# Performance work log

Hardware: AMD Instinct MI355X
Metric: run time of the kernel (lower is better)

## Reference

```python
import jax, jax.numpy as jnp
import numpy as np

B, T, D = 4, 2048, 1024
H, HS = 16, 64  # n_head, head_size


def setup_inputs() -> dict:
    key = jax.random.key(0)
    ks = jax.random.split(key, 6)
    s_in = 1.0 / np.sqrt(D)
    s_out = 1.0 / np.sqrt(H * HS)
    x = jax.random.normal(ks[0], (B, T, D), dtype=jnp.float32)
    Wq = jax.random.uniform(ks[1], (H, D, HS), jnp.float32, -s_in, s_in)
    Wk = jax.random.uniform(ks[2], (H, D, HS), jnp.float32, -s_in, s_in)
    Wv = jax.random.uniform(ks[3], (H, D, HS), jnp.float32, -s_in, s_in)
    Wo = jax.random.uniform(ks[4], (H * HS, D), jnp.float32, -s_out, s_out)
    bo = jax.random.uniform(ks[5], (D,), jnp.float32, -s_out, s_out)
    return {"x": x, "Wq": Wq, "Wk": Wk, "Wv": Wv, "Wo": Wo, "bo": bo}


def reference(x, Wq, Wk, Wv, Wo, bo):
    # per-head projections, batched across heads: [B,T,D] x [H,D,HS] -> [B,H,T,HS]
    q = jnp.einsum("btd,hde->bhte", x, Wq)
    k = jnp.einsum("btd,hde->bhte", x, Wk)
    v = jnp.einsum("btd,hde->bhte", x, Wv)
    scale = HS ** -0.5
    scores = jnp.einsum("bhqe,bhke->bhqk", q, k) * scale  # [B,H,T,T]
    causal = jnp.tril(jnp.ones((T, T), dtype=bool))
    scores = jnp.where(causal, scores, jnp.float32(-jnp.inf))
    attn = jax.nn.softmax(scores, axis=-1)
    out = jnp.einsum("bhqk,bhke->bhqe", attn, v)  # [B,H,T,HS]
    out = out.transpose(0, 2, 1, 3).reshape(B, T, H * HS)  # concat heads
    return out @ Wo + bo
```

## Files before the change

kernel.cpp:

```cpp
#include <hip/hip_runtime.h>

typedef __attribute__((ext_vector_type(8))) short short8v;
typedef __attribute__((ext_vector_type(4))) short short4v;
typedef __attribute__((ext_vector_type(4))) float floatx4;
typedef __attribute__((ext_vector_type(4))) unsigned uint4v;
typedef __attribute__((ext_vector_type(2))) unsigned long long ulong2v;

namespace {
constexpr int Bn = 4, Tn = 2048, Dn = 1024, Hn = 16, HSn = 64;
}

__device__ __forceinline__ short f2bf(float f) {
  unsigned u = __builtin_bit_cast(unsigned, f);
  u += 0x7fffu + ((u >> 16) & 1u);
  return (short)(u >> 16);
}

__device__ __forceinline__ unsigned pkbf2(float lo, float hi) {
  unsigned r;
  asm("v_cvt_pk_bf16_f32 %0, %1, %2" : "=v"(r) : "v"(lo), "v"(hi));
  return r;
}

typedef const __attribute__((address_space(1))) unsigned int guint_t;
typedef __attribute__((address_space(3))) unsigned int luint_t;

__device__ __forceinline__ void gload16(const void* g, void* l) {
  __builtin_amdgcn_global_load_lds((guint_t*)g, (luint_t*)l, 16, 0, 0);
}

__device__ __forceinline__ short8v rd8(const char* base, int row, int kel) {
  return *(const short8v*)(base + row * 128 + ((kel * 2) ^ ((row & 7) << 4)));
}

__global__ __launch_bounds__(256) void cvt_x_k(const float* __restrict__ x, short* __restrict__ xb) {
  const size_t i = ((size_t)blockIdx.x * 256 + threadIdx.x) * 8;
  const float4 a = *(const float4*)(x + i);
  const float4 b = *(const float4*)(x + i + 4);
  short8v o;
  o[0] = f2bf(a.x); o[1] = f2bf(a.y); o[2] = f2bf(a.z); o[3] = f2bf(a.w);
  o[4] = f2bf(b.x); o[5] = f2bf(b.y); o[6] = f2bf(b.z); o[7] = f2bf(b.w);
  *(short8v*)(xb + i) = o;
}

__global__ __launch_bounds__(256) void tr_w_k(const float* __restrict__ Wq, const float* __restrict__ Wk,
                                              const float* __restrict__ Wv, const float* __restrict__ Wo,
                                              short* __restrict__ wt, short* __restrict__ wot) {
  __shared__ float T[64][65];
  const int t = threadIdx.x;
  const int rr = t >> 2, c0 = (t & 3) * 4;
  const float* src;
  short* dst;
  if (blockIdx.x < 48) {
    const int ph = blockIdx.x;
    const int p = ph >> 4, h = ph & 15;
    const int dt = blockIdx.y;
    const float* W = p == 0 ? Wq : p == 1 ? Wk : Wv;
    src = W + (size_t)h * (Dn * HSn) + (size_t)(dt * 64 + rr) * HSn;
    dst = wt + ((size_t)p * 1024 + h * 64 + rr) * 1024 + dt * 64;
  } else {
    const int ktile = blockIdx.x - 48, ntile = blockIdx.y;
    src = Wo + (size_t)(ktile * 64 + rr) * Dn + ntile * 64;
    dst = wot + (size_t)(ntile * 64 + rr) * 1024 + ktile * 64;
  }
  #pragma unroll
  for (int q = 0; q < 4; ++q) {
    const float4 v = *(const float4*)(src + c0 + q * 16);
    T[rr][c0 + q * 16 + 0] = v.x; T[rr][c0 + q * 16 + 1] = v.y;
    T[rr][c0 + q * 16 + 2] = v.z; T[rr][c0 + q * 16 + 3] = v.w;
  }
  __syncthreads();
  #pragma unroll
  for (int q = 0; q < 4; ++q) {
    const int dl = c0 + q * 16;
    short4v ov = {f2bf(T[dl + 0][rr]), f2bf(T[dl + 1][rr]),
                  f2bf(T[dl + 2][rr]), f2bf(T[dl + 3][rr])};
    *(short4v*)(dst + dl) = ov;
  }
}

__device__ __forceinline__ void gemm_mainloop(const char* gA, const char* gB, char* As, char* Bs,
                                              floatx4 acc[4][4]) {
  const int tid = threadIdx.x;
  const int wv = tid >> 6, ln = tid & 63;
  const int wr = wv >> 1, wc = wv & 1;
  const int lr = ln >> 3, lg = ln & 7;
  const int fr = ln & 15, kq = ln >> 4;
  for (int kt = 0; kt < 16; ++kt) {
    __syncthreads();
    #pragma unroll
    for (int c = 0; c < 4; ++c) {
      const int r = wv * 32 + c * 8 + lr;
      const int sw = (lg * 16) ^ ((r & 7) * 16);
      gload16(gA + (size_t)r * 2048 + kt * 128 + sw, As + (wv * 32 + c * 8) * 128);
      gload16(gB + (size_t)r * 2048 + kt * 128 + sw, Bs + (wv * 32 + c * 8) * 128);
    }
    __syncthreads();
    #pragma unroll
    for (int kb = 0; kb < 2; ++kb) {
      const int k0 = kb * 32 + kq * 8;
      short8v af[4], bfr[4];
      #pragma unroll
      for (int i = 0; i < 4; ++i) af[i] = rd8(As, wr * 64 + i * 16 + fr, k0);
      #pragma unroll
      for (int j = 0; j < 4; ++j) bfr[j] = rd8(Bs, wc * 64 + j * 16 + fr, k0);
      #pragma unroll
      for (int i = 0; i < 4; ++i)
        #pragma unroll
        for (int j = 0; j < 4; ++j)
          acc[i][j] = __builtin_amdgcn_mfma_f32_16x16x32_bf16(af[i], bfr[j], acc[i][j], 0, 0, 0);
    }
  }
}

__global__ __launch_bounds__(256) void gemm_qkv_k(const short* __restrict__ xb, const short* __restrict__ wt,
                                                  short* __restrict__ qb, short* __restrict__ kb,
                                                  short* __restrict__ vb) {
  __shared__ __align__(16) char As[16384];
  __shared__ __align__(16) char Bs[16384];
  const int m0 = blockIdx.x * 128, n0 = blockIdx.y * 128;
  floatx4 acc[4][4];
  #pragma unroll
  for (int i = 0; i < 4; ++i)
    #pragma unroll
    for (int j = 0; j < 4; ++j) acc[i][j] = floatx4{0.f, 0.f, 0.f, 0.f};
  gemm_mainloop((const char*)xb + (size_t)m0 * 2048, (const char*)wt + (size_t)n0 * 2048, As, Bs, acc);

  const int tid = threadIdx.x, wv = tid >> 6, ln = tid & 63;
  const int wr = wv >> 1, wc = wv & 1;
  const int proj = n0 >> 10;
  const int b = m0 >> 11;
  const int rb_ = (ln >> 4) * 4, fc = ln & 15;
  if (proj < 2) {
    short* dst = proj == 0 ? qb : kb;
    const float sc = proj == 0 ? 0.18033688011112042f : 1.0f;
    #pragma unroll
    for (int i = 0; i < 4; ++i) {
      const int m = m0 + wr * 64 + i * 16 + rb_;
      #pragma unroll
      for (int j = 0; j < 4; ++j) {
        const int n = n0 + wc * 64 + j * 16 + fc;
        const int h = (n >> 6) & 15, e = n & 63;
        short* dp = dst + ((size_t)(b * 16 + h) * Tn + (m & 2047)) * 64 + e;
        #pragma unroll
        for (int r = 0; r < 4; ++r) dp[(size_t)r * 64] = f2bf(acc[i][j][r] * sc);
      }
    }
  } else {
    #pragma unroll
    for (int i = 0; i < 4; ++i) {
      const int m = m0 + wr * 64 + i * 16 + rb_;
      const int t0 = m & 2047;
      #pragma unroll
      for (int j = 0; j < 4; ++j) {
        const int n = n0 + wc * 64 + j * 16 + fc;
        const int h = (n >> 6) & 15, e = n & 63;
        short4v ov = {f2bf(acc[i][j][0]), f2bf(acc[i][j][1]),
                      f2bf(acc[i][j][2]), f2bf(acc[i][j][3])};
        *(short4v*)(vb + ((size_t)(b * 16 + h) * 64 + e) * Tn + t0) = ov;
      }
    }
  }
}

__global__ __launch_bounds__(256, 4) void attn_k(const short* __restrict__ qg, const short* __restrict__ kg,
                                                 const short* __restrict__ vg, short* __restrict__ og) {
  __shared__ __align__(16) char Ks[16384];
  __shared__ __align__(16) char Vs[16384];
  const int qt = gridDim.y - 1 - blockIdx.y;
  const int bh = blockIdx.x;
  const int tid = threadIdx.x, wv = tid >> 6, ln = tid & 63;
  const int lr = ln >> 3, lg = ln & 7;
  const int fr = ln & 15, kq = ln >> 4;
  const char* qbase = (const char*)qg + (size_t)bh * Tn * 128;
  const char* kbase = (const char*)kg + (size_t)bh * Tn * 128;
  const char* vbase = (const char*)vg + (size_t)bh * Tn * 128;

  #pragma unroll
  for (int c = 0; c < 2; ++c) {
    const int r = c * 32 + wv * 8 + lr;
    const int sw = (lg * 16) ^ ((r & 7) * 16);
    gload16(kbase + (size_t)r * 128 + sw, Ks + (c * 32 + wv * 8) * 128);
    gload16(vbase + (size_t)r * 4096 + sw, Vs + (c * 32 + wv * 8) * 128);
  }

  const char* qrow0 = qbase + (size_t)(qt * 128 + wv * 32) * 128;
  short8v qf[2][2];
  #pragma unroll
  for (int c = 0; c < 2; ++c)
    #pragma unroll
    for (int kb = 0; kb < 2; ++kb)
      qf[c][kb] = *(const short8v*)(qrow0 + (c * 16 + fr) * 128 + kb * 64 + kq * 16);

  short8v ones8;
  #pragma unroll
  for (int i = 0; i < 8; ++i) ones8[i] = (short)0x3F80;

  floatx4 ot[4][2];
  #pragma unroll
  for (int f = 0; f < 4; ++f) { ot[f][0] = floatx4{0.f,0.f,0.f,0.f}; ot[f][1] = floatx4{0.f,0.f,0.f,0.f}; }
  floatx4 lacc[2] = {floatx4{0.f,0.f,0.f,0.f}, floatx4{0.f,0.f,0.f,0.f}};
  float m_i[2] = {-1e30f, -1e30f};

  const int swz = (fr & 7) * 16;
  const int nkt = 2 * qt + 2;
  const int q0w = qt * 128 + wv * 32;
  __syncthreads();

  for (int kt = 0; kt < nkt; ++kt) {
    const int cur = kt & 1;
    if (kt + 1 < nkt) {
      #pragma unroll
      for (int c = 0; c < 2; ++c) {
        const int r = c * 32 + wv * 8 + lr;
        const int sw = (lg * 16) ^ ((r & 7) * 16);
        gload16(kbase + (size_t)((kt + 1) * 64 + r) * 128 + sw,
                Ks + (cur ^ 1) * 8192 + (c * 32 + wv * 8) * 128);
        gload16(vbase + (size_t)r * 4096 + (size_t)(kt + 1) * 128 + sw,
                Vs + (cur ^ 1) * 8192 + (c * 32 + wv * 8) * 128);
      }
    }
    if (kt * 64 <= q0w + 31) {
      const char* Ksc = Ks + cur * 8192;
      const char* Vsc = Vs + cur * 8192;
      floatx4 st[2][4];
      #pragma unroll
      for (int f = 0; f < 4; ++f) { st[0][f] = floatx4{0.f,0.f,0.f,0.f}; st[1][f] = floatx4{0.f,0.f,0.f,0.f}; }
      #pragma unroll
      for (int kb = 0; kb < 2; ++kb) {
        const int e0 = kb * 32 + kq * 8;
        #pragma unroll
        for (int f = 0; f < 4; ++f) {
          const short8v kf = rd8(Ksc, f * 16 + fr, e0);
          st[0][f] = __builtin_amdgcn_mfma_f32_16x16x32_bf16(kf, qf[0][kb], st[0][f], 0, 0, 0);
          st[1][f] = __builtin_amdgcn_mfma_f32_16x16x32_bf16(kf, qf[1][kb], st[1][f], 0, 0, 0);
        }
      }
      if (kt * 64 + 63 > q0w) {
        #pragma unroll
        for (int c = 0; c < 2; ++c) {
          const int q = q0w + c * 16 + fr;
          #pragma unroll
          for (int f = 0; f < 4; ++f)
            #pragma unroll
            for (int r = 0; r < 4; ++r)
              if (kt * 64 + f * 16 + kq * 4 + r > q) st[c][f][r] = -3.0e38f;
        }
      }
      float mx[2];
      #pragma unroll
      for (int c = 0; c < 2; ++c) {
        float v = fmaxf(fmaxf(st[c][0][0], st[c][0][1]), st[c][0][2]);
        v = fmaxf(fmaxf(v, st[c][0][3]), st[c][1][0]);
        v = fmaxf(fmaxf(v, st[c][1][1]), st[c][1][2]);
        v = fmaxf(fmaxf(v, st[c][1][3]), st[c][2][0]);
        v = fmaxf(fmaxf(v, st[c][2][1]), st[c][2][2]);
        v = fmaxf(fmaxf(v, st[c][2][3]), st[c][3][0]);
        v = fmaxf(fmaxf(v, st[c][3][1]), st[c][3][2]);
        v = fmaxf(v, st[c][3][3]);
        v = fmaxf(v, __shfl_xor(v, 16, 64));
        v = fmaxf(v, __shfl_xor(v, 32, 64));
        mx[c] = v;
      }
      const bool noresc = __all((mx[0] <= m_i[0] + 8.f) && (mx[1] <= m_i[1] + 8.f));
      if (!noresc) {
        #pragma unroll
        for (int c = 0; c < 2; ++c) {
          const float mn = fmaxf(m_i[c], mx[c]);
          const float al = exp2f(m_i[c] - mn);
          m_i[c] = mn;
          lacc[c] *= al;
          #pragma unroll
          for (int f = 0; f < 4; ++f) ot[f][c] *= al;
        }
      }
      short8v pbv[2][2];
      #pragma unroll
      for (int c = 0; c < 2; ++c)
        #pragma unroll
        for (int kb = 0; kb < 2; ++kb) {
          uint4v u;
          u[0] = pkbf2(exp2f(st[c][kb][0] - m_i[c]),     exp2f(st[c][kb][1] - m_i[c]));
          u[1] = pkbf2(exp2f(st[c][kb][2] - m_i[c]),     exp2f(st[c][kb][3] - m_i[c]));
          u[2] = pkbf2(exp2f(st[c][kb + 2][0] - m_i[c]), exp2f(st[c][kb + 2][1] - m_i[c]));
          u[3] = pkbf2(exp2f(st[c][kb + 2][2] - m_i[c]), exp2f(st[c][kb + 2][3] - m_i[c]));
          pbv[c][kb] = __builtin_bit_cast(short8v, u);
        }
      #pragma unroll
      for (int kb = 0; kb < 2; ++kb) {
        lacc[0] = __builtin_amdgcn_mfma_f32_16x16x32_bf16(ones8, pbv[0][kb], lacc[0], 0, 0, 0);
        lacc[1] = __builtin_amdgcn_mfma_f32_16x16x32_bf16(ones8, pbv[1][kb], lacc[1], 0, 0, 0);
      }
      #pragma unroll
      for (int kb = 0; kb < 2; ++kb) {
        const int blo = (kb * 32 + kq * 8) ^ swz;
        const int bhi = (kb * 32 + 64 + kq * 8) ^ swz;
        #pragma unroll
        for (int f = 0; f < 4; ++f) {
          const char* vrow = Vsc + (f * 16 + fr) * 128;
          ulong2v vv;
          vv[0] = *(const unsigned long long*)(vrow + blo);
          vv[1] = *(const unsigned long long*)(vrow + bhi);
          const short8v vf = __builtin_bit_cast(short8v, vv);
          ot[f][0] = __builtin_amdgcn_mfma_f32_16x16x32_bf16(vf, pbv[0][kb], ot[f][0], 0, 0, 0);
          ot[f][1] = __builtin_amdgcn_mfma_f32_16x16x32_bf16(vf, pbv[1][kb], ot[f][1], 0, 0, 0);
        }
      }
    }
    __syncthreads();
  }

  const int b = bh >> 4, h = bh & 15;
  #pragma unroll
  for (int c = 0; c < 2; ++c) {
    const float inv = 1.0f / lacc[c][0];
    const size_t t = (size_t)(b * Tn + qt * 128 + wv * 32 + c * 16 + fr);
    #pragma unroll
    for (int f = 0; f < 4; ++f) {
      uint2 o4 = {pkbf2(ot[f][c][0] * inv, ot[f][c][1] * inv),
                  pkbf2(ot[f][c][2] * inv, ot[f][c][3] * inv)};
      *(uint2*)(og + t * 1024 + h * 64 + f * 16 + kq * 4) = o4;
    }
  }
}

__global__ __launch_bounds__(256) void gemm_out_k(const short* __restrict__ ao, const short* __restrict__ wot,
                                                  const float* __restrict__ bo, float* __restrict__ out) {
  __shared__ __align__(16) char As[16384];
  __shared__ __align__(16) char Bs[16384];
  const int m0 = blockIdx.x * 128, n0 = blockIdx.y * 128;
  floatx4 acc[4][4];
  #pragma unroll
  for (int i = 0; i < 4; ++i)
    #pragma unroll
    for (int j = 0; j < 4; ++j) acc[i][j] = floatx4{0.f, 0.f, 0.f, 0.f};
  gemm_mainloop((const char*)ao + (size_t)m0 * 2048, (const char*)wot + (size_t)n0 * 2048, As, Bs, acc);

  const int tid = threadIdx.x, wv = tid >> 6, ln = tid & 63;
  const int wr = wv >> 1, wc = wv & 1;
  const int rb_ = (ln >> 4) * 4, fc = ln & 15;
  #pragma unroll
  for (int i = 0; i < 4; ++i) {
    const int m = m0 + wr * 64 + i * 16 + rb_;
    #pragma unroll
    for (int j = 0; j < 4; ++j) {
      const int n = n0 + wc * 64 + j * 16 + fc;
      const float bias = bo[n];
      #pragma unroll
      for (int r = 0; r < 4; ++r) out[(size_t)(m + r) * Dn + n] = acc[i][j][r] + bias;
    }
  }
}

extern "C" void kernel_launch(void* const* d_in, const int* in_sizes, int n_in,
                              void* d_out, int out_size, void* d_ws, size_t ws_size,
                              hipStream_t stream) {
  const float* x  = (const float*)d_in[0];
  const float* Wq = (const float*)d_in[1];
  const float* Wk = (const float*)d_in[2];
  const float* Wv = (const float*)d_in[3];
  const float* Wo = (const float*)d_in[4];
  const float* bo = (const float*)d_in[5];
  float* out = (float*)d_out;

  char* ws = (char*)d_ws;
  short* xb  = (short*)(ws);
  short* wt  = (short*)(ws + (16u << 20));
  short* wot = (short*)(ws + (22u << 20));
  short* qb  = (short*)(ws + (24u << 20));
  short* kb  = (short*)(ws + (40u << 20));
  short* vb  = (short*)(ws + (56u << 20));
  short* ao  = (short*)(ws + (72u << 20));

  cvt_x_k<<<4096, 256, 0, stream>>>(x, xb);
  tr_w_k<<<dim3(64, 16), 256, 0, stream>>>(Wq, Wk, Wv, Wo, wt, wot);
  gemm_qkv_k<<<dim3(64, 24), 256, 0, stream>>>(xb, wt, qb, kb, vb);
  attn_k<<<dim3(64, 16), 256, 0, stream>>>(qb, kb, vb, ao);
  gemm_out_k<<<dim3(64, 8), 256, 0, stream>>>(ao, wot, bo, out);
}
```

Baseline: 172.2 us.

## Merge prep kernels, stage V transpose through LDS, raise attention occupancy

Fuses the x conversion and the weight-transpose kernels into one launch using a flattened grid, which removes one kernel launch. In the QKV GEMM epilogue, V tiles are now staged through a swizzled shared buffer so each thread writes 16-byte contiguous rows of the transposed V, replacing scattered 8-byte stores. The attention kernel's launch_bounds min-blocks hint goes from 4 to 5, which can force register spilling.

```diff
diff --git a/kernel.cpp b/kernel.cpp
--- a/kernel.cpp
+++ b/kernel.cpp
@@ -33,35 +33,36 @@
   return *(const short8v*)(base + row * 128 + ((kel * 2) ^ ((row & 7) << 4)));
 }
 
-__global__ __launch_bounds__(256) void cvt_x_k(const float* __restrict__ x, short* __restrict__ xb) {
-  const size_t i = ((size_t)blockIdx.x * 256 + threadIdx.x) * 8;
-  const float4 a = *(const float4*)(x + i);
-  const float4 b = *(const float4*)(x + i + 4);
-  short8v o;
-  o[0] = f2bf(a.x); o[1] = f2bf(a.y); o[2] = f2bf(a.z); o[3] = f2bf(a.w);
-  o[4] = f2bf(b.x); o[5] = f2bf(b.y); o[6] = f2bf(b.z); o[7] = f2bf(b.w);
-  *(short8v*)(xb + i) = o;
-}
-
-__global__ __launch_bounds__(256) void tr_w_k(const float* __restrict__ Wq, const float* __restrict__ Wk,
+__global__ __launch_bounds__(256) void prep_k(const float* __restrict__ x,
+                                              const float* __restrict__ Wq, const float* __restrict__ Wk,
                                               const float* __restrict__ Wv, const float* __restrict__ Wo,
-                                              short* __restrict__ wt, short* __restrict__ wot) {
+                                              short* __restrict__ xb, short* __restrict__ wt,
+                                              short* __restrict__ wot) {
+  if (blockIdx.x >= 1024) {
+    const size_t i = ((size_t)(blockIdx.x - 1024) * 256 + threadIdx.x) * 8;
+    const float4 a = *(const float4*)(x + i);
+    const float4 b = *(const float4*)(x + i + 4);
+    short8v o;
+    o[0] = f2bf(a.x); o[1] = f2bf(a.y); o[2] = f2bf(a.z); o[3] = f2bf(a.w);
+    o[4] = f2bf(b.x); o[5] = f2bf(b.y); o[6] = f2bf(b.z); o[7] = f2bf(b.w);
+    *(short8v*)(xb + i) = o;
+    return;
+  }
   __shared__ float T[64][65];
+  const int bx = blockIdx.x & 63, by = blockIdx.x >> 6;
   const int t = threadIdx.x;
   const int rr = t >> 2, c0 = (t & 3) * 4;
   const float* src;
   short* dst;
-  if (blockIdx.x < 48) {
-    const int ph = blockIdx.x;
-    const int p = ph >> 4, h = ph & 15;
-    const int dt = blockIdx.y;
+  if (bx < 48) {
+    const int p = bx >> 4, h = bx & 15;
     const float* W = p == 0 ? Wq : p == 1 ? Wk : Wv;
-    src = W + (size_t)h * (Dn * HSn) + (size_t)(dt * 64 + rr) * HSn;
-    dst = wt + ((size_t)p * 1024 + h * 64 + rr) * 1024 + dt * 64;
+    src = W + (size_t)h * (Dn * HSn) + (size_t)(by * 64 + rr) * HSn;
+    dst = wt + ((size_t)p * 1024 + h * 64 + rr) * 1024 + by * 64;
   } else {
-    const int ktile = blockIdx.x - 48, ntile = blockIdx.y;
-    src = Wo + (size_t)(ktile * 64 + rr) * Dn + ntile * 64;
-    dst = wot + (size_t)(ntile * 64 + rr) * 1024 + ktile * 64;
+    const int ktile = bx - 48;
+    src = Wo + (size_t)(ktile * 64 + rr) * Dn + by * 64;
+    dst = wot + (size_t)(by * 64 + rr) * 1024 + ktile * 64;
   }
   #pragma unroll
   for (int q = 0; q < 4; ++q) {
@@ -116,8 +117,9 @@
 __global__ __launch_bounds__(256) void gemm_qkv_k(const short* __restrict__ xb, const short* __restrict__ wt,
                                                   short* __restrict__ qb, short* __restrict__ kb,
                                                   short* __restrict__ vb) {
-  __shared__ __align__(16) char As[16384];
-  __shared__ __align__(16) char Bs[16384];
+  __shared__ __align__(16) char S[32768];
+  char* As = S;
+  char* Bs = S + 16384;
   const int m0 = blockIdx.x * 128, n0 = blockIdx.y * 128;
   floatx4 acc[4][4];
   #pragma unroll
@@ -147,23 +149,33 @@
       }
     }
   } else {
+    __syncthreads();
     #pragma unroll
     for (int i = 0; i < 4; ++i) {
-      const int m = m0 + wr * 64 + i * 16 + rb_;
-      const int t0 = m & 2047;
+      const int ml = wr * 64 + i * 16 + rb_;
       #pragma unroll
       for (int j = 0; j < 4; ++j) {
-        const int n = n0 + wc * 64 + j * 16 + fc;
-        const int h = (n >> 6) & 15, e = n & 63;
+        const int nl = wc * 64 + j * 16 + fc;
         short4v ov = {f2bf(acc[i][j][0]), f2bf(acc[i][j][1]),
                       f2bf(acc[i][j][2]), f2bf(acc[i][j][3])};
-        *(short4v*)(vb + ((size_t)(b * 16 + h) * 64 + e) * Tn + t0) = ov;
-      }
-    }
-  }
-}
-
-__global__ __launch_bounds__(256, 4) void attn_k(const short* __restrict__ qg, const short* __restrict__ kg,
+        *(short4v*)(S + nl * 256 + ((ml * 2) ^ ((nl & 7) << 4))) = ov;
+      }
+    }
+    __syncthreads();
+    const int t00 = m0 & 2047;
+    #pragma unroll
+    for (int it = 0; it < 8; ++it) {
+      const int nl = it * 16 + (tid >> 4);
+      const int mc = (tid & 15) * 8;
+      const int n = n0 + nl;
+      const int h2 = (n >> 6) & 15, e = n & 63;
+      const uint4v vvv = *(const uint4v*)(S + nl * 256 + ((mc * 2) ^ ((nl & 7) << 4)));
+      *(uint4v*)(vb + ((size_t)(b * 16 + h2) * 64 + e) * Tn + t00 + mc) = vvv;
+    }
+  }
+}
+
+__global__ __launch_bounds__(256, 5) void attn_k(const short* __restrict__ qg, const short* __restrict__ kg,
                                                  const short* __restrict__ vg, short* __restrict__ og) {
   __shared__ __align__(16) char Ks[16384];
   __shared__ __align__(16) char Vs[16384];
@@ -326,8 +338,9 @@
 
 __global__ __launch_bounds__(256) void gemm_out_k(const short* __restrict__ ao, const short* __restrict__ wot,
                                                   const float* __restrict__ bo, float* __restrict__ out) {
-  __shared__ __align__(16) char As[16384];
-  __shared__ __align__(16) char Bs[16384];
+  __shared__ __align__(16) char S[32768];
+  char* As = S;
+  char* Bs = S + 16384;
   const int m0 = blockIdx.x * 128, n0 = blockIdx.y * 128;
   floatx4 acc[4][4];
   #pragma unroll
@@ -372,8 +385,7 @@
   short* vb  = (short*)(ws + (56u << 20));
   short* ao  = (short*)(ws + (72u << 20));
 
-  cvt_x_k<<<4096, 256, 0, stream>>>(x, xb);
-  tr_w_k<<<dim3(64, 16), 256, 0, stream>>>(Wq, Wk, Wv, Wo, wt, wot);
+  prep_k<<<5120, 256, 0, stream>>>(x, Wq, Wk, Wv, Wo, xb, wt, wot);
   gemm_qkv_k<<<dim3(64, 24), 256, 0, stream>>>(xb, wt, qb, kb, vb);
   attn_k<<<dim3(64, 16), 256, 0, stream>>>(qb, kb, vb, ao);
   gemm_out_k<<<dim3(64, 8), 256, 0, stream>>>(ao, wot, bo, out);
```

Measured after the change: 301.5 us. 1.75x slower.
